# Kernel optimization log

Measured on AMD Instinct MI355X. Metric: run time of the kernel, lower is better.

## Reference

```python
import jax, jax.numpy as jnp
import numpy as np

# Dims: batch B, channels C, spatial HxW; modes: weight spatial (32, 17) ('count' mode)
B, C, H, W = 8, 128, 128, 128
M_ROWS, M_COLS = 32, 17          # weight spatial size = [n_modes[0], n_modes[1]//2 + 1]
L_TOP = 17                       # n_modes[0]//2 + 1  -> rows [:17]
R_BOT = 15                       # n_modes[0] - L_TOP -> rows [-15:]


def setup_inputs() -> dict:
    key = jax.random.key(0)
    k1, k2, k3 = jax.random.split(key, 3)
    scale = C ** (-2)  # matches torch: scale * rand(..., cfloat) -> re/im ~ U[0, scale)
    X = jax.random.normal(k1, (B, C, H, W), dtype=jnp.float32)
    linear_re = scale * jax.random.uniform(k2, (C, C, M_ROWS, M_COLS), dtype=jnp.float32)
    linear_im = scale * jax.random.uniform(k3, (C, C, M_ROWS, M_COLS), dtype=jnp.float32)
    return {"X": X, "linear_re": linear_re, "linear_im": linear_im}


def _block(w_eff, xf):
    # w_eff: (C, C, m0, m1) complex, xf: (B, C, m0, m1) complex -> (B, C, m0, m1)
    return jnp.einsum('ctxy,btxy->bcxy', w_eff, xf)


def reference(X, linear_re, linear_im):
    Wc = linear_re + 1j * linear_im                       # (C, C, 32, 17) complex64
    # skew-Hermitian weight: linear - conj(linear).transpose(1, 0)
    W_eff = Wc - jnp.conj(jnp.swapaxes(Wc, 0, 1))
    Xf = jnp.fft.rfftn(X, axes=(-2, -1), norm='forward')  # (B, C, H, W//2+1) complex
    Y = jnp.zeros(Xf.shape, dtype=jnp.complex64)
    # corner block 1: low positive row frequencies
    Y = Y.at[:, :, :L_TOP, :M_COLS].set(
        _block(W_eff[:, :, :L_TOP, :], Xf[:, :, :L_TOP, :M_COLS]))
    # corner block 2: negative row frequencies
    Y = Y.at[:, :, -R_BOT:, :M_COLS].set(
        _block(W_eff[:, :, -R_BOT:, :], Xf[:, :, -R_BOT:, :M_COLS]))
    out = jnp.fft.irfftn(Y, s=(H, W), axes=(-2, -1), norm='forward')
    return out.astype(X.dtype)
```

## Files before the change

### kernel.cpp

```cpp
#include <hip/hip_runtime.h>
#include <math.h>

#define PI_F 3.14159265358979323846f

constexpr int NM = 544;

constexpr size_t OFF_F1 = 0;
constexpr size_t OFF_F2 = 17408;
constexpr size_t OFF_G  = 37888;
constexpr size_t OFF_CT = 70656;
constexpr size_t OFF_XF = 88064;
constexpr size_t OFF_YS = 4544512;
constexpr size_t OFF_YP = 9000960;

__global__ __launch_bounds__(256) void k_tab(float* __restrict__ F1, float* __restrict__ F2,
                                             float2* __restrict__ G, float2* __restrict__ CT) {
  const int t0 = blockIdx.x * 256 + threadIdx.x;
  const int N = gridDim.x * 256;
  const float inv = 1.0f / 16384.0f;
  for (int i = t0; i < 128 * 17; i += N) {
    int x = i / 17, r = i - 17 * x;
    float s, c; sincosf(-2.f * PI_F * (float)((x * r) & 127) / 128.f, &s, &c);
    F1[x * 34 + 2 * r] = c * inv; F1[x * 34 + 2 * r + 1] = s * inv;
  }
  for (int i = t0; i < 128 * 20; i += N) {
    int y = i / 20, k = i - 20 * y;
    if (k >= 17) { F2[y * 40 + 2 * k] = 0.f; F2[y * 40 + 2 * k + 1] = 0.f; }
    else {
      float s, c; sincosf(-2.f * PI_F * (float)((y * k) & 127) / 128.f, &s, &c);
      F2[y * 40 + 2 * k] = c; F2[y * 40 + 2 * k + 1] = s;
    }
  }
  for (int i = t0; i < 32 * 128; i += N) {
    int r = i >> 7, x = i & 127;
    int f = (r < 17) ? r : r + 96;
    float s, c; sincosf(2.f * PI_F * (float)((f * x) & 127) / 128.f, &s, &c);
    G[i] = make_float2(c, s);
  }
  for (int i = t0; i < 17 * 128; i += N) {
    int k = i >> 7;
    float w = k ? 2.f : 1.f;
    float s, c; sincosf(2.f * PI_F * (float)((k * (i & 127)) & 127) / 128.f, &s, &c);
    CT[i] = make_float2(w * c, w * s);
  }
}

__global__ __launch_bounds__(256) void k_fwd(const float* __restrict__ X,
                                             const float* __restrict__ F1,
                                             const float* __restrict__ F2,
                                             float2* __restrict__ Xf) {
  __shared__ float2 tmp[128][17];
  __shared__ float2 red[128][17];
  const int tid = threadIdx.x;
  const int bt = blockIdx.x;
  const int y = tid & 127;
  const int g = tid >> 7;

  float2 acc[17];
#pragma unroll
  for (int r = 0; r < 17; ++r) acc[r] = make_float2(0.f, 0.f);
  const float* xp = X + (size_t)bt * 16384 + y;
#pragma unroll 4
  for (int xi = 0; xi < 64; ++xi) {
    int x = g * 64 + xi;
    float v = xp[(size_t)x * 128];
    const float* f = F1 + x * 34;
#pragma unroll
    for (int r = 0; r < 17; ++r) {
      acc[r].x = fmaf(v, f[2 * r], acc[r].x);
      acc[r].y = fmaf(v, f[2 * r + 1], acc[r].y);
    }
  }
  if (g) {
#pragma unroll
    for (int r = 0; r < 17; ++r) red[y][r] = acc[r];
  }
  __syncthreads();
  if (!g) {
#pragma unroll
    for (int r = 0; r < 17; ++r) {
      float2 o = red[y][r];
      tmp[y][r] = make_float2(acc[r].x + o.x, acc[r].y + o.y);
    }
  }
  __syncthreads();

  const int lane = tid & 63;
  const int w = tid >> 6;
  const int r = lane & 31;
  const int yh = lane >> 5;
  const int r2 = (r < 17) ? r : 32 - r;
  const float sgn = (r < 17) ? 1.f : -1.f;
  const int ky0 = w * 5;
  const int nky = (w == 3) ? 2 : 5;
  float2 a2[5];
#pragma unroll
  for (int i = 0; i < 5; ++i) a2[i] = make_float2(0.f, 0.f);
  const float* f2b = F2 + 2 * ky0 + yh * 40;
  for (int yl = 0; yl < 64; ++yl) {
    float2 tv = tmp[2 * yl + yh][r2];
    float tvy = tv.y * sgn;
    const float* f = f2b + yl * 80;
#pragma unroll
    for (int i = 0; i < 5; ++i) {
      float cr = f[2 * i], ci = f[2 * i + 1];
      a2[i].x = fmaf(tv.x, cr, fmaf(-tvy, ci, a2[i].x));
      a2[i].y = fmaf(tv.x, ci, fmaf(tvy, cr, a2[i].y));
    }
  }
#pragma unroll
  for (int i = 0; i < 5; ++i) {
    a2[i].x += __shfl_xor(a2[i].x, 32);
    a2[i].y += __shfl_xor(a2[i].y, 32);
  }
  if (lane < 32) {
    for (int i = 0; i < nky; ++i)
      Xf[(size_t)bt * NM + r * 17 + ky0 + i] = a2[i];
  }
}

__global__ __launch_bounds__(576) void k_mix(const float* __restrict__ Wre,
                                             const float* __restrict__ Wim,
                                             const float2* __restrict__ Xf,
                                             float2* __restrict__ Yp) {
  const int m = threadIdx.x;
  if (m >= NM) return;
  const int c = blockIdx.x & 127;
  const int q = blockIdx.x >> 7;
  const int chunk = q & 3;
  const int b0 = (q >> 2) * 4;
  float2 acc[4];
#pragma unroll
  for (int b = 0; b < 4; ++b) acc[b] = make_float2(0.f, 0.f);
  const int t0 = chunk * 32;
#pragma unroll 2
  for (int tt = 0; tt < 32; ++tt) {
    const int t = t0 + tt;
    float wr = Wre[(size_t)(c * 128 + t) * NM + m] - Wre[(size_t)(t * 128 + c) * NM + m];
    float wi = Wim[(size_t)(c * 128 + t) * NM + m] + Wim[(size_t)(t * 128 + c) * NM + m];
#pragma unroll
    for (int b = 0; b < 4; ++b) {
      float2 xv = Xf[(size_t)((b0 + b) * 128 + t) * NM + m];
      acc[b].x = fmaf(wr, xv.x, fmaf(-wi, xv.y, acc[b].x));
      acc[b].y = fmaf(wr, xv.y, fmaf(wi, xv.x, acc[b].y));
    }
  }
#pragma unroll
  for (int b = 0; b < 4; ++b)
    Yp[(size_t)chunk * 1024 * NM + (size_t)((b0 + b) * 128 + c) * NM + m] = acc[b];
}

__global__ __launch_bounds__(256) void k_red(const float2* __restrict__ Yp,
                                             float2* __restrict__ Ys) {
  int i = blockIdx.x * 256 + threadIdx.x;
  if (i >= 1024 * NM) return;
  int bc = i / NM, m = i - bc * NM;
  int r = m / 17, ky = m - r * 17;
  float2 s = make_float2(0.f, 0.f);
#pragma unroll
  for (int ch = 0; ch < 4; ++ch) {
    float2 v = Yp[(size_t)ch * 1024 * NM + i];
    s.x += v.x; s.y += v.y;
  }
  Ys[(size_t)bc * NM + ky * 32 + r] = s;
}

__global__ __launch_bounds__(256) void k_invB(const float* __restrict__ Ys,
                                              const float2* __restrict__ G,
                                              float2* __restrict__ Z) {
  const int tid = threadIdx.x;
  const int lane = tid & 63;
  const int bc = __builtin_amdgcn_readfirstlane(blockIdx.x * 2 + (tid >> 7));
  const int xh = __builtin_amdgcn_readfirstlane((tid >> 6) & 1);
  const int x = xh * 64 + lane;
  float2 g[32];
#pragma unroll
  for (int r = 0; r < 32; ++r) g[r] = G[r * 128 + x];
  const float* yb = Ys + (size_t)bc * (NM * 2);
  float2* zb = Z + (size_t)bc * (17 * 128) + x;
  for (int ky = 0; ky < 17; ++ky) {
    const float* yk = yb + ky * 64;
    float zr = 0.f, zi = 0.f;
#pragma unroll
    for (int r = 0; r < 32; ++r) {
      float ar = yk[2 * r], ai = yk[2 * r + 1];
      zr = fmaf(ar, g[r].x, fmaf(-ai, g[r].y, zr));
      zi = fmaf(ar, g[r].y, fmaf(ai, g[r].x, zi));
    }
    zb[ky * 128] = make_float2(zr, zi);
  }
}

__global__ __launch_bounds__(256) void k_invC(const float* __restrict__ Z,
                                              const float2* __restrict__ CT,
                                              float* __restrict__ out) {
  const int tid = threadIdx.x;
  const int yy = tid & 127;
  const int xh = __builtin_amdgcn_readfirstlane(tid >> 7);
  const int bc = blockIdx.x;
  float2 ct[17];
#pragma unroll
  for (int k = 0; k < 17; ++k) ct[k] = CT[k * 128 + yy];
  const float* zb = Z + (size_t)bc * (17 * 128 * 2);
  float* op = out + (size_t)bc * 16384;
#pragma unroll 2
  for (int xi = 0; xi < 64; ++xi) {
    int x = xh * 64 + xi;
    const float* zp = zb + 2 * x;
    float s = 0.f;
#pragma unroll
    for (int k = 0; k < 17; ++k) {
      float zr = zp[k * 256], zi = zp[k * 256 + 1];
      s = fmaf(zr, ct[k].x, fmaf(-zi, ct[k].y, s));
    }
    op[x * 128 + yy] = s;
  }
}

extern "C" void kernel_launch(void* const* d_in, const int* in_sizes, int n_in,
                              void* d_out, int out_size, void* d_ws, size_t ws_size,
                              hipStream_t stream) {
  const float* X   = (const float*)d_in[0];
  const float* Wre = (const float*)d_in[1];
  const float* Wim = (const float*)d_in[2];
  float* out = (float*)d_out;

  char* ws = (char*)d_ws;
  float*  F1 = (float*)(ws + OFF_F1);
  float*  F2 = (float*)(ws + OFF_F2);
  float2* G  = (float2*)(ws + OFF_G);
  float2* CT = (float2*)(ws + OFF_CT);
  float2* Xf = (float2*)(ws + OFF_XF);
  float2* Ys = (float2*)(ws + OFF_YS);
  float2* Yp = (float2*)(ws + OFF_YP);
  float2* Z  = Yp;

  k_tab <<<32, 256, 0, stream>>>(F1, F2, G, CT);
  k_fwd <<<1024, 256, 0, stream>>>(X, F1, F2, Xf);
  k_mix <<<1024, 576, 0, stream>>>(Wre, Wim, Xf, Yp);
  k_red <<<2176, 256, 0, stream>>>(Yp, Ys);
  k_invB<<<512, 256, 0, stream>>>((const float*)Ys, G, Z);
  k_invC<<<1024, 256, 0, stream>>>((const float*)Z, CT, out);
}
```

Before: 390.0 us.

## Restructure forward DFT work split across waves and split inverse row pass per block

The forward kernel stage one now gives each wave a group of row frequencies (4 per wave, plus the 17th on wave 0). The twiddle table is transposed so lanes read it with wave-uniform addresses, which removes the cross-half reduction and one barrier. The second-stage twiddles are staged into shared memory and read as float4. The inverse row kernel now handles one (b,c) per block with the two half-blocks splitting the ky range, doubling the grid. This trades more redundant loads of X per wave and some imbalance on wave 0 for fewer registers and better occupancy.

```diff
diff --git a/kernel.cpp b/kernel.cpp
--- a/kernel.cpp
+++ b/kernel.cpp
@@ -5,23 +5,23 @@
 
 constexpr int NM = 544;
 
-constexpr size_t OFF_F1 = 0;
-constexpr size_t OFF_F2 = 17408;
-constexpr size_t OFF_G  = 37888;
-constexpr size_t OFF_CT = 70656;
-constexpr size_t OFF_XF = 88064;
-constexpr size_t OFF_YS = 4544512;
-constexpr size_t OFF_YP = 9000960;
-
-__global__ __launch_bounds__(256) void k_tab(float* __restrict__ F1, float* __restrict__ F2,
+constexpr size_t OFF_F1T = 0;
+constexpr size_t OFF_F2  = 17408;
+constexpr size_t OFF_G   = 37888;
+constexpr size_t OFF_CT  = 70656;
+constexpr size_t OFF_XF  = 88064;
+constexpr size_t OFF_YS  = 4544512;
+constexpr size_t OFF_YP  = 9000960;
+
+__global__ __launch_bounds__(256) void k_tab(float* __restrict__ F1T, float* __restrict__ F2,
                                              float2* __restrict__ G, float2* __restrict__ CT) {
   const int t0 = blockIdx.x * 256 + threadIdx.x;
   const int N = gridDim.x * 256;
   const float inv = 1.0f / 16384.0f;
-  for (int i = t0; i < 128 * 17; i += N) {
-    int x = i / 17, r = i - 17 * x;
+  for (int i = t0; i < 17 * 128; i += N) {
+    int r = i >> 7, x = i & 127;
     float s, c; sincosf(-2.f * PI_F * (float)((x * r) & 127) / 128.f, &s, &c);
-    F1[x * 34 + 2 * r] = c * inv; F1[x * 34 + 2 * r + 1] = s * inv;
+    F1T[2 * i] = c * inv; F1T[2 * i + 1] = s * inv;
   }
   for (int i = t0; i < 128 * 20; i += N) {
     int y = i / 20, k = i - 20 * y;
@@ -46,67 +46,88 @@
 }
 
 __global__ __launch_bounds__(256) void k_fwd(const float* __restrict__ X,
-                                             const float* __restrict__ F1,
-                                             const float* __restrict__ F2,
+                                             const float* __restrict__ F1T,
+                                             const float* __restrict__ F2G,
                                              float2* __restrict__ Xf) {
-  __shared__ float2 tmp[128][17];
-  __shared__ float2 red[128][17];
+  __shared__ float tmpL[128 * 38];
+  __shared__ float f2s[128 * 40];
   const int tid = threadIdx.x;
   const int bt = blockIdx.x;
-  const int y = tid & 127;
-  const int g = tid >> 7;
-
-  float2 acc[17];
-#pragma unroll
-  for (int r = 0; r < 17; ++r) acc[r] = make_float2(0.f, 0.f);
-  const float* xp = X + (size_t)bt * 16384 + y;
-#pragma unroll 4
-  for (int xi = 0; xi < 64; ++xi) {
-    int x = g * 64 + xi;
-    float v = xp[(size_t)x * 128];
-    const float* f = F1 + x * 34;
-#pragma unroll
-    for (int r = 0; r < 17; ++r) {
-      acc[r].x = fmaf(v, f[2 * r], acc[r].x);
-      acc[r].y = fmaf(v, f[2 * r + 1], acc[r].y);
-    }
-  }
-  if (g) {
-#pragma unroll
-    for (int r = 0; r < 17; ++r) red[y][r] = acc[r];
+
+  {
+    const float4* src = (const float4*)F2G;
+    float4* dst = (float4*)f2s;
+    for (int i = tid; i < 1280; i += 256) dst[i] = src[i];
+  }
+
+  const int wid = __builtin_amdgcn_readfirstlane(tid >> 6);
+  const int lane = tid & 63;
+  const bool w0 = (wid == 0);
+  const int r0 = wid * 4;
+
+  for (int yh = 0; yh < 2; ++yh) {
+    const int y = yh * 64 + lane;
+    float2 acc[5];
+#pragma unroll
+    for (int i = 0; i < 5; ++i) acc[i] = make_float2(0.f, 0.f);
+    const float* xp = X + (size_t)bt * 16384 + y;
+    for (int xc = 0; xc < 32; ++xc) {
+      const float* xq = xp + xc * 512;
+      float v0 = xq[0], v1 = xq[128], v2 = xq[256], v3 = xq[384];
+#pragma unroll
+      for (int i = 0; i < 4; ++i) {
+        const float* t = F1T + ((r0 + i) << 8) + (xc << 3);
+        acc[i].x = fmaf(v0, t[0], acc[i].x); acc[i].y = fmaf(v0, t[1], acc[i].y);
+        acc[i].x = fmaf(v1, t[2], acc[i].x); acc[i].y = fmaf(v1, t[3], acc[i].y);
+        acc[i].x = fmaf(v2, t[4], acc[i].x); acc[i].y = fmaf(v2, t[5], acc[i].y);
+        acc[i].x = fmaf(v3, t[6], acc[i].x); acc[i].y = fmaf(v3, t[7], acc[i].y);
+      }
+      if (w0) {
+        const float* t = F1T + (16 << 8) + (xc << 3);
+        acc[4].x = fmaf(v0, t[0], acc[4].x); acc[4].y = fmaf(v0, t[1], acc[4].y);
+        acc[4].x = fmaf(v1, t[2], acc[4].x); acc[4].y = fmaf(v1, t[3], acc[4].y);
+        acc[4].x = fmaf(v2, t[4], acc[4].x); acc[4].y = fmaf(v2, t[5], acc[4].y);
+        acc[4].x = fmaf(v3, t[6], acc[4].x); acc[4].y = fmaf(v3, t[7], acc[4].y);
+      }
+    }
+#pragma unroll
+    for (int i = 0; i < 4; ++i) {
+      tmpL[y * 38 + 2 * (r0 + i)]     = acc[i].x;
+      tmpL[y * 38 + 2 * (r0 + i) + 1] = acc[i].y;
+    }
+    if (w0) { tmpL[y * 38 + 32] = acc[4].x; tmpL[y * 38 + 33] = acc[4].y; }
   }
   __syncthreads();
-  if (!g) {
-#pragma unroll
-    for (int r = 0; r < 17; ++r) {
-      float2 o = red[y][r];
-      tmp[y][r] = make_float2(acc[r].x + o.x, acc[r].y + o.y);
-    }
-  }
-  __syncthreads();
-
-  const int lane = tid & 63;
-  const int w = tid >> 6;
+
   const int r = lane & 31;
   const int yh = lane >> 5;
   const int r2 = (r < 17) ? r : 32 - r;
   const float sgn = (r < 17) ? 1.f : -1.f;
-  const int ky0 = w * 5;
-  const int nky = (w == 3) ? 2 : 5;
+  const int ky0 = wid * 4;
   float2 a2[5];
 #pragma unroll
   for (int i = 0; i < 5; ++i) a2[i] = make_float2(0.f, 0.f);
-  const float* f2b = F2 + 2 * ky0 + yh * 40;
+  const float* f2p = f2s + yh * 40 + 2 * ky0;
+  const float* tp  = tmpL + yh * 38 + 2 * r2;
   for (int yl = 0; yl < 64; ++yl) {
-    float2 tv = tmp[2 * yl + yh][r2];
-    float tvy = tv.y * sgn;
-    const float* f = f2b + yl * 80;
-#pragma unroll
-    for (int i = 0; i < 5; ++i) {
-      float cr = f[2 * i], ci = f[2 * i + 1];
-      a2[i].x = fmaf(tv.x, cr, fmaf(-tvy, ci, a2[i].x));
-      a2[i].y = fmaf(tv.x, ci, fmaf(tvy, cr, a2[i].y));
-    }
+    float2 tv = *(const float2*)tp;
+    float tx = tv.x, ts = tv.y * sgn;
+    float4 c01 = *(const float4*)(f2p);
+    float4 c23 = *(const float4*)(f2p + 4);
+    a2[0].x = fmaf(tx, c01.x, fmaf(-ts, c01.y, a2[0].x));
+    a2[0].y = fmaf(tx, c01.y, fmaf( ts, c01.x, a2[0].y));
+    a2[1].x = fmaf(tx, c01.z, fmaf(-ts, c01.w, a2[1].x));
+    a2[1].y = fmaf(tx, c01.w, fmaf( ts, c01.z, a2[1].y));
+    a2[2].x = fmaf(tx, c23.x, fmaf(-ts, c23.y, a2[2].x));
+    a2[2].y = fmaf(tx, c23.y, fmaf( ts, c23.x, a2[2].y));
+    a2[3].x = fmaf(tx, c23.z, fmaf(-ts, c23.w, a2[3].x));
+    a2[3].y = fmaf(tx, c23.w, fmaf( ts, c23.z, a2[3].y));
+    if (w0) {
+      float2 c4 = *(const float2*)(f2p + 32);
+      a2[4].x = fmaf(tx, c4.x, fmaf(-ts, c4.y, a2[4].x));
+      a2[4].y = fmaf(tx, c4.y, fmaf( ts, c4.x, a2[4].y));
+    }
+    f2p += 80; tp += 76;
   }
 #pragma unroll
   for (int i = 0; i < 5; ++i) {
@@ -114,8 +135,10 @@
     a2[i].y += __shfl_xor(a2[i].y, 32);
   }
   if (lane < 32) {
-    for (int i = 0; i < nky; ++i)
-      Xf[(size_t)bt * NM + r * 17 + ky0 + i] = a2[i];
+    float2* xo = Xf + (size_t)bt * NM + r * 17 + ky0;
+#pragma unroll
+    for (int i = 0; i < 4; ++i) xo[i] = a2[i];
+    if (w0) xo[16] = a2[4];
   }
 }
 
@@ -170,15 +193,18 @@
                                               float2* __restrict__ Z) {
   const int tid = threadIdx.x;
   const int lane = tid & 63;
-  const int bc = __builtin_amdgcn_readfirstlane(blockIdx.x * 2 + (tid >> 7));
   const int xh = __builtin_amdgcn_readfirstlane((tid >> 6) & 1);
+  const int p  = __builtin_amdgcn_readfirstlane(tid >> 7);
   const int x = xh * 64 + lane;
+  const int bc = blockIdx.x;
   float2 g[32];
 #pragma unroll
   for (int r = 0; r < 32; ++r) g[r] = G[r * 128 + x];
   const float* yb = Ys + (size_t)bc * (NM * 2);
   float2* zb = Z + (size_t)bc * (17 * 128) + x;
-  for (int ky = 0; ky < 17; ++ky) {
+#pragma unroll
+  for (int i = 0; i < 8; ++i) {
+    const int ky = 2 * i + p;
     const float* yk = yb + ky * 64;
     float zr = 0.f, zi = 0.f;
 #pragma unroll
@@ -188,6 +214,17 @@
       zi = fmaf(ar, g[r].y, fmaf(ai, g[r].x, zi));
     }
     zb[ky * 128] = make_float2(zr, zi);
+  }
+  if (p == 0) {
+    const float* yk = yb + 16 * 64;
+    float zr = 0.f, zi = 0.f;
+#pragma unroll
+    for (int r = 0; r < 32; ++r) {
+      float ar = yk[2 * r], ai = yk[2 * r + 1];
+      zr = fmaf(ar, g[r].x, fmaf(-ai, g[r].y, zr));
+      zi = fmaf(ar, g[r].y, fmaf(ai, g[r].x, zi));
+    }
+    zb[16 * 128] = make_float2(zr, zi);
   }
 }
 
@@ -226,19 +263,19 @@
   float* out = (float*)d_out;
 
   char* ws = (char*)d_ws;
-  float*  F1 = (float*)(ws + OFF_F1);
-  float*  F2 = (float*)(ws + OFF_F2);
-  float2* G  = (float2*)(ws + OFF_G);
-  float2* CT = (float2*)(ws + OFF_CT);
-  float2* Xf = (float2*)(ws + OFF_XF);
-  float2* Ys = (float2*)(ws + OFF_YS);
-  float2* Yp = (float2*)(ws + OFF_YP);
-  float2* Z  = Yp;
-
-  k_tab <<<32, 256, 0, stream>>>(F1, F2, G, CT);
-  k_fwd <<<1024, 256, 0, stream>>>(X, F1, F2, Xf);
+  float*  F1T = (float*)(ws + OFF_F1T);
+  float*  F2  = (float*)(ws + OFF_F2);
+  float2* G   = (float2*)(ws + OFF_G);
+  float2* CT  = (float2*)(ws + OFF_CT);
+  float2* Xf  = (float2*)(ws + OFF_XF);
+  float2* Ys  = (float2*)(ws + OFF_YS);
+  float2* Yp  = (float2*)(ws + OFF_YP);
+  float2* Z   = Yp;
+
+  k_tab <<<32, 256, 0, stream>>>(F1T, F2, G, CT);
+  k_fwd <<<1024, 256, 0, stream>>>(X, F1T, F2, Xf);
   k_mix <<<1024, 576, 0, stream>>>(Wre, Wim, Xf, Yp);
   k_red <<<2176, 256, 0, stream>>>(Yp, Ys);
-  k_invB<<<512, 256, 0, stream>>>((const float*)Ys, G, Z);
+  k_invB<<<1024, 256, 0, stream>>>((const float*)Ys, G, Z);
   k_invC<<<1024, 256, 0, stream>>>((const float*)Z, CT, out);
 }
```

New measurement: 334.6 us. -14.2%, faster.
